# Kernel tuning notes

Hardware: AMD Instinct MI355X
Metric: run time of the kernel (lower is better)

## Reference

```python
import jax, jax.numpy as jnp
import numpy as np

B, L, E, D, H, N_ENT = 64, 50, 50, 100, 100, 200000


def setup_inputs() -> dict:
    key = jax.random.key(0)
    ks = jax.random.split(key, 12)
    neighbor_ids = jax.random.randint(ks[0], (B, L, E), 0, N_ENT)
    # 0/1 adjacency; mimic GraphConstructer: symmetric with self-loops
    adj = jax.random.randint(ks[1], (B, L, E, E), 0, 2).astype(jnp.int32)
    adj = jnp.maximum(adj, adj.transpose(0, 1, 3, 2))
    adj = jnp.maximum(adj, jnp.eye(E, dtype=jnp.int32))
    s = 0.1  # ~ 1/sqrt(D) init scale
    emb = jax.random.normal(ks[2], (N_ENT, D), jnp.float32) * s
    Wq = jax.random.normal(ks[3], (D, H), jnp.float32) * s
    bq = jax.random.normal(ks[4], (H,), jnp.float32) * s
    Wk = jax.random.normal(ks[5], (D, H), jnp.float32) * s
    bk = jax.random.normal(ks[6], (H,), jnp.float32) * s
    Wv = jax.random.normal(ks[7], (D, H), jnp.float32) * s
    bv = jax.random.normal(ks[8], (H,), jnp.float32) * s
    Ws = jax.random.normal(ks[9], (D, H), jnp.float32) * s
    bs = jax.random.normal(ks[10], (H,), jnp.float32) * s
    return {"neighbor_ids": neighbor_ids, "adj": adj, "emb": emb,
            "Wq": Wq, "bq": bq, "Wk": Wk, "bk": bk,
            "Wv": Wv, "bv": bv, "Ws": Ws, "bs": bs}


def reference(neighbor_ids, adj, emb, Wq, bq, Wk, bk, Wv, bv, Ws, bs):
    b, l, e = neighbor_ids.shape
    d = emb.shape[1]
    h = Wq.shape[1]
    # embedding gather: [B,L,E,D] -> [G,E,D], G = B*L graphs
    x = emb[neighbor_ids].reshape(b * l, e, d)
    a = adj.reshape(b * l, e, e)
    # TransformerConv (heads=1): q,k,v linear with bias
    q = x @ Wq + bq
    k = x @ Wk + bk
    v = x @ Wv + bv
    scores = jnp.einsum('gid,gjd->gij', q, k) / jnp.sqrt(jnp.asarray(h, x.dtype))
    # edge (j -> i) exists when adj[j, i] != 0; target i attends over sources j
    mask = a.transpose(0, 2, 1) != 0  # mask[g, i, j]
    neg = jnp.finfo(scores.dtype).min
    attn = jax.nn.softmax(jnp.where(mask, scores, neg), axis=-1)
    # nodes with no incoming edge aggregate to zero (PyG softmax/scatter semantics)
    attn = jnp.where(mask.any(-1, keepdims=True), attn, jnp.zeros((), attn.dtype))
    agg = jnp.einsum('gij,gjd->gid', attn, v)
    out = agg + x @ Ws + bs  # root/skip connection with bias
    # take center node (index 0) of each ego-graph -> [B, L, H]
    return out.reshape(b, l, e, h)[:, :, 0, :]
```

## Files before the change

### kernel.cpp

```cpp
#include <hip/hip_runtime.h>
#include <hip/hip_bf16.h>
#include <math.h>

#define E_N 50
#define D_N 100
#define H_N 100
#define XS_LD 102

__device__ __forceinline__ float bf2f(unsigned int s16) {
    return __uint_as_float(s16 << 16);
}

__device__ __forceinline__ unsigned short f2bf(float f) {
    unsigned int u = __float_as_uint(f);
    unsigned int r = (u + 0x7FFFu + ((u >> 16) & 1u)) >> 16;
    return (unsigned short)r;
}

template <bool F32>
__device__ __forceinline__ float ldx(const void* p, int i) {
    if (F32) return reinterpret_cast<const float*>(p)[i];
    return bf2f(reinterpret_cast<const unsigned short*>(p)[i]);
}

template <bool F32>
__device__ __forceinline__ float4 ld4(const void* p, long long i4) {
    if (F32) return reinterpret_cast<const float4*>(p)[i4];
    uint2 v = reinterpret_cast<const uint2*>(p)[i4];
    float4 f;
    f.x = bf2f(v.x & 0xFFFFu);
    f.y = bf2f(v.x >> 16);
    f.z = bf2f(v.y & 0xFFFFu);
    f.w = bf2f(v.y >> 16);
    return f;
}

__device__ __forceinline__ int detect_f32(const void* emb, int tid, int* flag_s) {
    if (tid < 64) {
        unsigned short hw = reinterpret_cast<const unsigned short*>(emb)[tid * 2];
        float v = bf2f(hw);
        float a = fabsf(v);
        int sane = (v == 0.f) || (a >= 1e-4f && a <= 8.0f);
        unsigned long long ball = __ballot(sane);
        if (tid == 0) *flag_s = (__popcll(ball) < 32) ? 1 : 0;
    }
    __syncthreads();
    return *flag_s;
}

template <bool F32>
__device__ __forceinline__ void prep_core(const void* Wq, const void* bq,
                                          const void* Wk, const void* bv,
                                          const void* bs,
                                          float* Mt, float* c, float* b2,
                                          int blk, int t) {
    if (blk < D_N) {
        if (t < D_N) {
            float acc = 0.f;
            #pragma unroll 10
            for (int h = 0; h < H_N; ++h)
                acc = fmaf(ldx<F32>(Wk, t * H_N + h), ldx<F32>(Wq, blk * H_N + h), acc);
            Mt[blk * D_N + t] = acc;
        }
    } else {
        if (t < D_N) {
            float acc = 0.f;
            #pragma unroll 10
            for (int h = 0; h < H_N; ++h)
                acc = fmaf(ldx<F32>(Wk, t * H_N + h), ldx<F32>(bq, h), acc);
            c[t] = acc;
            b2[t] = ldx<F32>(bs, t) + ldx<F32>(bv, t);
        }
    }
}

__global__ __launch_bounds__(128)
void prep_kernel(const void* __restrict__ emb,
                 const void* __restrict__ Wq, const void* __restrict__ bq,
                 const void* __restrict__ Wk, const void* __restrict__ bv,
                 const void* __restrict__ bs,
                 float* __restrict__ Mt, float* __restrict__ c,
                 float* __restrict__ b2) {
    __shared__ int flag_s;
    int t = threadIdx.x;
    int f32 = detect_f32(emb, t, &flag_s);
    if (f32) prep_core<true>(Wq, bq, Wk, bv, bs, Mt, c, b2, blockIdx.x, t);
    else     prep_core<false>(Wq, bq, Wk, bv, bs, Mt, c, b2, blockIdx.x, t);
}

template <bool F32>
__device__ __forceinline__ void graph_core(
    int g, int lane,
    const int* __restrict__ nbr, const int* __restrict__ adj,
    const void* __restrict__ emb,
    const void* __restrict__ Wv, const void* __restrict__ Ws,
    const void* __restrict__ bv,
    const float* __restrict__ Mt, const float* __restrict__ c,
    const float* __restrict__ b2, void* __restrict__ out,
    unsigned short* xs, float* x0s, int* ids, int* msk,
    float* us, float* ssc, float* attns, float* ys, float* den_s)
{
    if (lane < E_N) ids[lane] = nbr[g * E_N + lane];
    __syncthreads();

    unsigned int* xw = reinterpret_cast<unsigned int*>(xs);

    float4 bufA[10];
    #pragma unroll
    for (int k = 0; k < 10; ++k) {
        int i = lane + 64 * k;
        int j = i / 25, q = i - j * 25;
        bufA[k] = ld4<F32>(emb, (long long)ids[j] * 25 + q);
    }
    int mk = (lane < E_N) ? adj[(size_t)g * (E_N * E_N) + lane * E_N] : 0;

    float4 bufB[10];
    #pragma unroll
    for (int k = 0; k < 10; ++k) {
        int i = lane + 64 * (k + 10);
        if (i < E_N * 25) {
            int j = i / 25, q = i - j * 25;
            bufB[k] = ld4<F32>(emb, (long long)ids[j] * 25 + q);
        }
    }

    #pragma unroll
    for (int k = 0; k < 10; ++k) {
        int i = lane + 64 * k;
        int j = i / 25, q = i - j * 25;
        float4 f = bufA[k];
        xw[j * (XS_LD / 2) + 2 * q]     = (unsigned int)f2bf(f.x) | ((unsigned int)f2bf(f.y) << 16);
        xw[j * (XS_LD / 2) + 2 * q + 1] = (unsigned int)f2bf(f.z) | ((unsigned int)f2bf(f.w) << 16);
    }
    if (lane < 25) {
        float4 f = bufA[0];
        x0s[4 * lane + 0] = f.x; x0s[4 * lane + 1] = f.y;
        x0s[4 * lane + 2] = f.z; x0s[4 * lane + 3] = f.w;
    }
    #pragma unroll
    for (int k = 0; k < 10; ++k) {
        int i = lane + 64 * (k + 10);
        if (i < E_N * 25) {
            int j = i / 25, q = i - j * 25;
            float4 f = bufB[k];
            xw[j * (XS_LD / 2) + 2 * q]     = (unsigned int)f2bf(f.x) | ((unsigned int)f2bf(f.y) << 16);
            xw[j * (XS_LD / 2) + 2 * q + 1] = (unsigned int)f2bf(f.z) | ((unsigned int)f2bf(f.w) << 16);
        }
    }
    if (lane < E_N) msk[lane] = mk;
    __syncthreads();

    #pragma unroll
    for (int rep = 0; rep < 2; ++rep) {
        int d = lane + 64 * rep;
        if (d < D_N) {
            float acc = c[d];
            #pragma unroll 10
            for (int e = 0; e < D_N; ++e)
                acc = fmaf(Mt[e * D_N + d], x0s[e], acc);
            us[d] = acc;
        }
    }
    __syncthreads();

    if (lane < E_N) {
        const unsigned int* xr = xw + lane * (XS_LD / 2);
        float acc = 0.f;
        #pragma unroll 10
        for (int d2 = 0; d2 < D_N / 2; ++d2) {
            unsigned int w = xr[d2];
            acc = fmaf(bf2f(w & 0xFFFFu), us[2 * d2], acc);
            acc = fmaf(bf2f(w >> 16),     us[2 * d2 + 1], acc);
        }
        ssc[lane] = acc * 0.1f;
    }
    __syncthreads();

    if (lane < E_N) {
        float m = -3.0e38f;
        #pragma unroll 10
        for (int j = 0; j < E_N; ++j)
            if (msk[j]) m = fmaxf(m, ssc[j]);
        attns[lane] = msk[lane] ? __expf(ssc[lane] - m) : 0.f;
    }
    __syncthreads();

    {
        float den = 0.f;
        #pragma unroll 10
        for (int j = 0; j < E_N; ++j) den += attns[j];
        float inv = den > 0.f ? 1.0f / den : 0.f;
        #pragma unroll
        for (int rep = 0; rep < 2; ++rep) {
            int d = lane + 64 * rep;
            if (d < D_N) {
                float acc = 0.f;
                #pragma unroll 10
                for (int j = 0; j < E_N; ++j)
                    acc = fmaf(attns[j], bf2f(xs[j * XS_LD + d]), acc);
                ys[d] = acc * inv;
            }
        }
        if (lane == 0) *den_s = den;
    }
    __syncthreads();

    {
        float sneg = (*den_s > 0.f) ? 0.f : 1.f;
        #pragma unroll
        for (int rep = 0; rep < 2; ++rep) {
            int h = lane + 64 * rep;
            if (h < H_N) {
                float acc = b2[h] - sneg * ldx<F32>(bv, h);
                #pragma unroll 10
                for (int d = 0; d < D_N; ++d) {
                    acc = fmaf(ys[d],  ldx<F32>(Wv, d * H_N + h), acc);
                    acc = fmaf(x0s[d], ldx<F32>(Ws, d * H_N + h), acc);
                }
                size_t o = (size_t)g * H_N + h;
                if (F32) reinterpret_cast<float*>(out)[o] = acc;
                else     reinterpret_cast<unsigned short*>(out)[o] = f2bf(acc);
            }
        }
    }
}

__global__ __launch_bounds__(64)
void graph_enc_kernel(const int* __restrict__ nbr,
                      const int* __restrict__ adj,
                      const void* __restrict__ emb,
                      const void* __restrict__ Wv, const void* __restrict__ Ws,
                      const void* __restrict__ bv,
                      const float* __restrict__ Mt, const float* __restrict__ c,
                      const float* __restrict__ b2,
                      void* __restrict__ out)
{
    __shared__ unsigned short xs[E_N * XS_LD];
    __shared__ float x0s[D_N];
    __shared__ int   ids[E_N];
    __shared__ int   msk[E_N];
    __shared__ float us[D_N];
    __shared__ float ssc[E_N];
    __shared__ float attns[E_N];
    __shared__ float ys[D_N];
    __shared__ float den_s;
    __shared__ int   flag_s;

    const int lane = threadIdx.x;
    const int g    = blockIdx.x;

    int f32 = detect_f32(emb, lane, &flag_s);
    if (f32)
        graph_core<true>(g, lane, nbr, adj, emb, Wv, Ws, bv, Mt, c, b2, out,
                         xs, x0s, ids, msk, us, ssc, attns, ys, &den_s);
    else
        graph_core<false>(g, lane, nbr, adj, emb, Wv, Ws, bv, Mt, c, b2, out,
                          xs, x0s, ids, msk, us, ssc, attns, ys, &den_s);
}

extern "C" void kernel_launch(void* const* d_in, const int* in_sizes, int n_in,
                              void* d_out, int out_size, void* d_ws, size_t ws_size,
                              hipStream_t stream) {
    const int* nbr = (const int*)d_in[0];
    const int* adj = (const int*)d_in[1];
    const void* emb = d_in[2];
    const void* Wq  = d_in[3];
    const void* bq  = d_in[4];
    const void* Wk  = d_in[5];
    const void* Wv  = d_in[7];
    const void* bv  = d_in[8];
    const void* Ws  = d_in[9];
    const void* bs  = d_in[10];

    float* Mt = (float*)d_ws;
    float* c  = Mt + D_N * D_N;
    float* b2 = c + D_N;

    const int G = in_sizes[0] / E_N;

    prep_kernel<<<D_N + 1, 128, 0, stream>>>(emb, Wq, bq, Wk, bv, bs, Mt, c, b2);
    graph_enc_kernel<<<G, 64, 0, stream>>>(nbr, adj, emb, Wv, Ws, bv,
                                           Mt, c, b2, d_out);
}
```

Before: 195.9 us.

## Split graph encoder into query, attention and output projection kernels

```diff
diff --git a/kernel.cpp b/kernel.cpp
--- a/kernel.cpp
+++ b/kernel.cpp
@@ -5,7 +5,7 @@
 #define E_N 50
 #define D_N 100
 #define H_N 100
-#define XS_LD 102
+#define XS_LDW 51
 
 __device__ __forceinline__ float bf2f(unsigned int s16) {
     return __uint_as_float(s16 << 16);
@@ -49,61 +49,68 @@
 }
 
 template <bool F32>
-__device__ __forceinline__ void prep_core(const void* Wq, const void* bq,
-                                          const void* Wk, const void* bv,
-                                          const void* bs,
-                                          float* Mt, float* c, float* b2,
-                                          int blk, int t) {
-    if (blk < D_N) {
-        if (t < D_N) {
-            float acc = 0.f;
-            #pragma unroll 10
-            for (int h = 0; h < H_N; ++h)
-                acc = fmaf(ldx<F32>(Wk, t * H_N + h), ldx<F32>(Wq, blk * H_N + h), acc);
-            Mt[blk * D_N + t] = acc;
-        }
-    } else {
-        if (t < D_N) {
-            float acc = 0.f;
-            #pragma unroll 10
-            for (int h = 0; h < H_N; ++h)
-                acc = fmaf(ldx<F32>(Wk, t * H_N + h), ldx<F32>(bq, h), acc);
-            c[t] = acc;
-            b2[t] = ldx<F32>(bs, t) + ldx<F32>(bv, t);
-        }
-    }
-}
-
-__global__ __launch_bounds__(128)
-void prep_kernel(const void* __restrict__ emb,
-                 const void* __restrict__ Wq, const void* __restrict__ bq,
-                 const void* __restrict__ Wk, const void* __restrict__ bv,
-                 const void* __restrict__ bs,
-                 float* __restrict__ Mt, float* __restrict__ c,
-                 float* __restrict__ b2) {
+__device__ __forceinline__ void qu_core(int g, int tt, int act,
+    const int* __restrict__ nbr, const void* __restrict__ emb,
+    const void* __restrict__ Wq, const void* __restrict__ bq,
+    const void* __restrict__ Wk, float* __restrict__ U, float* q0s)
+{
+    int row = 0;
+    if (act) row = __builtin_amdgcn_readfirstlane(nbr[g * E_N]);
+
+    if (act && tt < H_N) {
+        float acc = ldx<F32>(bq, tt);
+        #pragma unroll 10
+        for (int d = 0; d < D_N; ++d)
+            acc = fmaf(ldx<F32>(emb, row * D_N + d), ldx<F32>(Wq, d * H_N + tt), acc);
+        q0s[tt] = acc;
+    }
+    __syncthreads();
+
+    if (act && tt < D_N) {
+        float acc = 0.f;
+        #pragma unroll
+        for (int hq = 0; hq < D_N / 4; ++hq) {
+            float4 w = ld4<F32>(Wk, (long long)tt * (H_N / 4) + hq);
+            const float4 q = reinterpret_cast<const float4*>(q0s)[hq];
+            acc = fmaf(w.x, q.x, acc);
+            acc = fmaf(w.y, q.y, acc);
+            acc = fmaf(w.z, q.z, acc);
+            acc = fmaf(w.w, q.w, acc);
+        }
+        U[(size_t)g * D_N + tt] = acc;
+    }
+}
+
+__global__ __launch_bounds__(256)
+void qu_kernel(const int* __restrict__ nbr, const void* __restrict__ emb,
+               const void* __restrict__ Wq, const void* __restrict__ bq,
+               const void* __restrict__ Wk, float* __restrict__ U, int G)
+{
+    __shared__ float q0s[2][H_N] __attribute__((aligned(16)));
     __shared__ int flag_s;
-    int t = threadIdx.x;
+    const int t = threadIdx.x;
+    const int sub = t >> 7, tt = t & 127;
+    const int g = blockIdx.x * 2 + sub;
+    const int act = (g < G);
     int f32 = detect_f32(emb, t, &flag_s);
-    if (f32) prep_core<true>(Wq, bq, Wk, bv, bs, Mt, c, b2, blockIdx.x, t);
-    else     prep_core<false>(Wq, bq, Wk, bv, bs, Mt, c, b2, blockIdx.x, t);
-}
-
-template <bool F32>
-__device__ __forceinline__ void graph_core(
-    int g, int lane,
+    if (f32) qu_core<true>(g, tt, act, nbr, emb, Wq, bq, Wk, U, q0s[sub]);
+    else     qu_core<false>(g, tt, act, nbr, emb, Wq, bq, Wk, U, q0s[sub]);
+}
+
+template <bool F32>
+__device__ __forceinline__ void graph_core(int g, int lane,
     const int* __restrict__ nbr, const int* __restrict__ adj,
-    const void* __restrict__ emb,
-    const void* __restrict__ Wv, const void* __restrict__ Ws,
-    const void* __restrict__ bv,
-    const float* __restrict__ Mt, const float* __restrict__ c,
-    const float* __restrict__ b2, void* __restrict__ out,
-    unsigned short* xs, float* x0s, int* ids, int* msk,
-    float* us, float* ssc, float* attns, float* ys, float* den_s)
-{
+    const void* __restrict__ emb, const float* __restrict__ U,
+    float* __restrict__ Y,
+    unsigned int* xw, int* ids, int* msk, float* us, float* ssc, float* attns)
+{
+    int mk = (lane < E_N) ? adj[(size_t)g * (E_N * E_N) + lane * E_N] : 0;
+    float4 uv;
+    if (lane < 25)
+        uv = reinterpret_cast<const float4*>(U + (size_t)g * D_N)[lane];
+
     if (lane < E_N) ids[lane] = nbr[g * E_N + lane];
     __syncthreads();
-
-    unsigned int* xw = reinterpret_cast<unsigned int*>(xs);
 
     float4 bufA[10];
     #pragma unroll
@@ -112,8 +119,6 @@
         int j = i / 25, q = i - j * 25;
         bufA[k] = ld4<F32>(emb, (long long)ids[j] * 25 + q);
     }
-    int mk = (lane < E_N) ? adj[(size_t)g * (E_N * E_N) + lane * E_N] : 0;
-
     float4 bufB[10];
     #pragma unroll
     for (int k = 0; k < 10; ++k) {
@@ -124,18 +129,16 @@
         }
     }
 
+    if (lane < E_N) msk[lane] = mk;
+    if (lane < 25) reinterpret_cast<float4*>(us)[lane] = uv;
+
     #pragma unroll
     for (int k = 0; k < 10; ++k) {
         int i = lane + 64 * k;
         int j = i / 25, q = i - j * 25;
         float4 f = bufA[k];
-        xw[j * (XS_LD / 2) + 2 * q]     = (unsigned int)f2bf(f.x) | ((unsigned int)f2bf(f.y) << 16);
-        xw[j * (XS_LD / 2) + 2 * q + 1] = (unsigned int)f2bf(f.z) | ((unsigned int)f2bf(f.w) << 16);
-    }
-    if (lane < 25) {
-        float4 f = bufA[0];
-        x0s[4 * lane + 0] = f.x; x0s[4 * lane + 1] = f.y;
-        x0s[4 * lane + 2] = f.z; x0s[4 * lane + 3] = f.w;
+        xw[j * XS_LDW + 2 * q]     = (unsigned int)f2bf(f.x) | ((unsigned int)f2bf(f.y) << 16);
+        xw[j * XS_LDW + 2 * q + 1] = (unsigned int)f2bf(f.z) | ((unsigned int)f2bf(f.w) << 16);
     }
     #pragma unroll
     for (int k = 0; k < 10; ++k) {
@@ -143,28 +146,14 @@
         if (i < E_N * 25) {
             int j = i / 25, q = i - j * 25;
             float4 f = bufB[k];
-            xw[j * (XS_LD / 2) + 2 * q]     = (unsigned int)f2bf(f.x) | ((unsigned int)f2bf(f.y) << 16);
-            xw[j * (XS_LD / 2) + 2 * q + 1] = (unsigned int)f2bf(f.z) | ((unsigned int)f2bf(f.w) << 16);
-        }
-    }
-    if (lane < E_N) msk[lane] = mk;
-    __syncthreads();
-
-    #pragma unroll
-    for (int rep = 0; rep < 2; ++rep) {
-        int d = lane + 64 * rep;
-        if (d < D_N) {
-            float acc = c[d];
-            #pragma unroll 10
-            for (int e = 0; e < D_N; ++e)
-                acc = fmaf(Mt[e * D_N + d], x0s[e], acc);
-            us[d] = acc;
+            xw[j * XS_LDW + 2 * q]     = (unsigned int)f2bf(f.x) | ((unsigned int)f2bf(f.y) << 16);
+            xw[j * XS_LDW + 2 * q + 1] = (unsigned int)f2bf(f.z) | ((unsigned int)f2bf(f.w) << 16);
         }
     }
     __syncthreads();
 
     if (lane < E_N) {
-        const unsigned int* xr = xw + lane * (XS_LD / 2);
+        const unsigned int* xr = xw + lane * XS_LDW;
         float acc = 0.f;
         #pragma unroll 10
         for (int d2 = 0; d2 < D_N / 2; ++d2) {
@@ -189,73 +178,81 @@
         float den = 0.f;
         #pragma unroll 10
         for (int j = 0; j < E_N; ++j) den += attns[j];
-        float inv = den > 0.f ? 1.0f / den : 0.f;
+        float inv = 1.0f / den;
         #pragma unroll
         for (int rep = 0; rep < 2; ++rep) {
             int d = lane + 64 * rep;
             if (d < D_N) {
                 float acc = 0.f;
                 #pragma unroll 10
-                for (int j = 0; j < E_N; ++j)
-                    acc = fmaf(attns[j], bf2f(xs[j * XS_LD + d]), acc);
-                ys[d] = acc * inv;
+                for (int j = 0; j < E_N; ++j) {
+                    unsigned int w = xw[j * XS_LDW + (d >> 1)];
+                    float xv = bf2f((d & 1) ? (w >> 16) : (w & 0xFFFFu));
+                    acc = fmaf(attns[j], xv, acc);
+                }
+                Y[(size_t)g * D_N + d] = acc * inv;
             }
         }
-        if (lane == 0) *den_s = den;
-    }
-    __syncthreads();
-
-    {
-        float sneg = (*den_s > 0.f) ? 0.f : 1.f;
-        #pragma unroll
-        for (int rep = 0; rep < 2; ++rep) {
-            int h = lane + 64 * rep;
-            if (h < H_N) {
-                float acc = b2[h] - sneg * ldx<F32>(bv, h);
-                #pragma unroll 10
-                for (int d = 0; d < D_N; ++d) {
-                    acc = fmaf(ys[d],  ldx<F32>(Wv, d * H_N + h), acc);
-                    acc = fmaf(x0s[d], ldx<F32>(Ws, d * H_N + h), acc);
-                }
-                size_t o = (size_t)g * H_N + h;
-                if (F32) reinterpret_cast<float*>(out)[o] = acc;
-                else     reinterpret_cast<unsigned short*>(out)[o] = f2bf(acc);
-            }
-        }
     }
 }
 
 __global__ __launch_bounds__(64)
-void graph_enc_kernel(const int* __restrict__ nbr,
-                      const int* __restrict__ adj,
-                      const void* __restrict__ emb,
-                      const void* __restrict__ Wv, const void* __restrict__ Ws,
-                      const void* __restrict__ bv,
-                      const float* __restrict__ Mt, const float* __restrict__ c,
-                      const float* __restrict__ b2,
-                      void* __restrict__ out)
-{
-    __shared__ unsigned short xs[E_N * XS_LD];
-    __shared__ float x0s[D_N];
+void graph_kernel(const int* __restrict__ nbr, const int* __restrict__ adj,
+                  const void* __restrict__ emb, const float* __restrict__ U,
+                  float* __restrict__ Y)
+{
+    __shared__ unsigned int xw[E_N * XS_LDW];
     __shared__ int   ids[E_N];
     __shared__ int   msk[E_N];
-    __shared__ float us[D_N];
+    __shared__ float us[D_N] __attribute__((aligned(16)));
     __shared__ float ssc[E_N];
     __shared__ float attns[E_N];
-    __shared__ float ys[D_N];
-    __shared__ float den_s;
     __shared__ int   flag_s;
 
     const int lane = threadIdx.x;
-    const int g    = blockIdx.x;
-
+    const int g = blockIdx.x;
     int f32 = detect_f32(emb, lane, &flag_s);
-    if (f32)
-        graph_core<true>(g, lane, nbr, adj, emb, Wv, Ws, bv, Mt, c, b2, out,
-                         xs, x0s, ids, msk, us, ssc, attns, ys, &den_s);
-    else
-        graph_core<false>(g, lane, nbr, adj, emb, Wv, Ws, bv, Mt, c, b2, out,
-                          xs, x0s, ids, msk, us, ssc, attns, ys, &den_s);
+    if (f32) graph_core<true>(g, lane, nbr, adj, emb, U, Y, xw, ids, msk, us, ssc, attns);
+    else     graph_core<false>(g, lane, nbr, adj, emb, U, Y, xw, ids, msk, us, ssc, attns);
+}
+
+template <bool F32>
+__device__ __forceinline__ void out_core(int g, int tt, int act,
+    const int* __restrict__ nbr, const void* __restrict__ emb,
+    const void* __restrict__ Wv, const void* __restrict__ Ws,
+    const void* __restrict__ bv, const void* __restrict__ bs,
+    const float* __restrict__ Y, void* __restrict__ out)
+{
+    if (!act) return;
+    int row = __builtin_amdgcn_readfirstlane(nbr[g * E_N]);
+    if (tt < H_N) {
+        float acc = ldx<F32>(bs, tt) + ldx<F32>(bv, tt);
+        const float* yg = Y + (size_t)g * D_N;
+        #pragma unroll 10
+        for (int d = 0; d < D_N; ++d) {
+            acc = fmaf(yg[d],                        ldx<F32>(Wv, d * H_N + tt), acc);
+            acc = fmaf(ldx<F32>(emb, row * D_N + d), ldx<F32>(Ws, d * H_N + tt), acc);
+        }
+        size_t o = (size_t)g * H_N + tt;
+        if (F32) reinterpret_cast<float*>(out)[o] = acc;
+        else     reinterpret_cast<unsigned short*>(out)[o] = f2bf(acc);
+    }
+}
+
+__global__ __launch_bounds__(256)
+void out_kernel(const int* __restrict__ nbr, const void* __restrict__ emb,
+                const void* __restrict__ Wv, const void* __restrict__ Ws,
+                const void* __restrict__ bv, const void* __restrict__ bs,
+                const float* __restrict__ Y, void* __restrict__ out, int G)
+{
+    __shared__ int flag_s;
+    const int t = threadIdx.x;
+    const int sub = t >> 7, tt = t & 127;
+    const int g = blockIdx.x * 2 + sub;
+    const int act = (g < G);
+    int f32 = detect_f32(emb, t, &flag_s);
+    if (f32) out_core<true>(g, tt, act, nbr, emb, Wv, Ws, bv, bs, Y, out);
+    else     out_core<false>(g, tt, act, nbr, emb, Wv, Ws, bv, bs, Y, out);
 }
 
 extern "C" void kernel_launch(void* const* d_in, const int* in_sizes, int n_in,
@@ -272,13 +269,11 @@
     const void* Ws  = d_in[9];
     const void* bs  = d_in[10];
 
-    float* Mt = (float*)d_ws;
-    float* c  = Mt + D_N * D_N;
-    float* b2 = c + D_N;
-
     const int G = in_sizes[0] / E_N;
-
-    prep_kernel<<<D_N + 1, 128, 0, stream>>>(emb, Wq, bq, Wk, bv, bs, Mt, c, b2);
-    graph_enc_kernel<<<G, 64, 0, stream>>>(nbr, adj, emb, Wv, Ws, bv,
-                                           Mt, c, b2, d_out);
-}
+    float* U = (float*)d_ws;
+    float* Y = U + (size_t)G * D_N;
+
+    qu_kernel<<<(G + 1) / 2, 256, 0, stream>>>(nbr, emb, Wq, bq, Wk, U, G);
+    graph_kernel<<<G, 64, 0, stream>>>(nbr, adj, emb, U, Y);
+    out_kernel<<<(G + 1) / 2, 256, 0, stream>>>(nbr, emb, Wv, Ws, bv, bs, Y, d_out, G);
+}
```

After: 209.1 us. 6.7% more time.
